# Kernel optimization log

Measured on AMD Instinct MI355X. Metric: run time of the kernel, lower is better.

Reference implementation:

```python
import jax, jax.numpy as jnp
import numpy as np


def setup_inputs() -> dict:
    key = jax.random.key(0)
    kq, kk, kv = jax.random.split(key, 3)
    B, M, QT, KVT, H = 2, 16, 2048, 2048, 128
    q = jax.random.normal(kq, (B, M, QT, H), dtype=jnp.float32)
    k = jax.random.normal(kk, (B, M, KVT, H), dtype=jnp.float32)
    v = jax.random.normal(kv, (B, M, KVT, H), dtype=jnp.float32)
    return {"q": q, "k": k, "v": v}


def reference(q, k, v):
    # QKBmm: broadcast-multiply + sum == einsum contraction over H.
    # NOTE: original module applies NO 1/sqrt(H) scaling.
    score = jnp.einsum("bmqh,bmkh->bmqk", q, k)  # [B,M,QT,KVT]
    score = jax.nn.softmax(score, axis=-1)
    # SVBmm: broadcast-multiply + sum over KVT.
    out = jnp.einsum("bmqk,bmkh->bmqh", score, v)  # [B,M,QT,H]
    return out
```

## Files before the change

### kernel.cpp

```cpp
#include <hip/hip_runtime.h>
#include <hip/hip_bf16.h>
#include <math.h>


#define HD     128
#define QTL    2048
#define KVTL   2048
#define NHEAD  32
#define KVBLK  64
#define NKT    (KVTL / KVBLK)
#define QBLKB  128
#define TILE_BYTES 32768
#define WS_NEEDED ((size_t)NHEAD * NKT * TILE_BYTES)

using f32x4  = __attribute__((ext_vector_type(4))) float;
using f32x16 = __attribute__((ext_vector_type(16))) float;
using f16x8  = __attribute__((ext_vector_type(8))) _Float16;
using f16x2  = __attribute__((ext_vector_type(2))) _Float16;
using i32x2  = __attribute__((ext_vector_type(2))) int;
using i32x4  = __attribute__((ext_vector_type(4))) int;
using bf16x8 = __attribute__((ext_vector_type(8))) __bf16;
using bf16x4 = __attribute__((ext_vector_type(4))) __bf16;

#define NK_CHUNK (NHEAD * NKT * 64 * 16)
#define NV_CHUNK (NHEAD * NKT * 8 * 128)

__global__ __launch_bounds__(256) void sdpa_prep(const float* __restrict__ kg,
                                                 const float* __restrict__ vg,
                                                 char* __restrict__ ws)
{
    const int idx = blockIdx.x * 256 + threadIdx.x;
    if (idx < NK_CHUNK) {
        const int s    = idx & 15;
        const int r    = (idx >> 4) & 63;
        const int kt   = (idx >> 10) & 31;
        const int head = idx >> 15;
        const int c    = s ^ (r & 15);
        const float* src = kg + ((size_t)head * KVTL + kt * 64 + r) * HD + c * 8;
        float4 a = *(const float4*)src;
        float4 b = *(const float4*)(src + 4);
        f16x8 h8;
        h8[0] = (_Float16)a.x; h8[1] = (_Float16)a.y;
        h8[2] = (_Float16)a.z; h8[3] = (_Float16)a.w;
        h8[4] = (_Float16)b.x; h8[5] = (_Float16)b.y;
        h8[6] = (_Float16)b.z; h8[7] = (_Float16)b.w;
        char* base = ws + (size_t)(head * NKT + kt) * TILE_BYTES;
        *(f16x8*)(base + r * 256 + s * 16) = h8;
    } else if (idx < NK_CHUNK + NV_CHUNK) {
        const int j    = idx - NK_CHUNK;
        const int h    = j & 127;
        const int c    = (j >> 7) & 7;
        const int kt   = (j >> 10) & 31;
        const int head = j >> 15;
        const int rr   = h & 63;
        const int u    = h >> 6;
        const int s    = (u * 8 + c) ^ (rr & 15);
        const float* src = vg + ((size_t)head * KVTL + kt * 64 + c * 8) * HD + h;
        f16x8 o;
        #pragma unroll
        for (int i = 0; i < 8; ++i)
            o[i] = (_Float16)src[(size_t)i * HD];
        char* base = ws + (size_t)(head * NKT + kt) * TILE_BYTES;
        *(f16x8*)(base + 16384 + rr * 256 + s * 16) = o;
    }
}

__device__ __forceinline__ void stage_tile(const char* __restrict__ g,
                                           char* lds, int t)
{
    #pragma unroll
    for (int j = 0; j < 8; ++j) {
        __builtin_amdgcn_global_load_lds(
            (const __attribute__((address_space(1))) void*)(g + j * 4096 + t * 16),
            (__attribute__((address_space(3))) void*)(lds + j * 4096 + t * 16),
            16, 0, 0);
    }
}

__global__ __launch_bounds__(256, 2) void sdpa_fwd(const float* __restrict__ qg,
                                                   const char* __restrict__ ws,
                                                   float* __restrict__ og)
{
    const int head  = blockIdx.y;
    const int qblk  = blockIdx.x * QBLKB;
    const float* qh = qg + (size_t)head * QTL * HD;
    const char*  wh = ws + (size_t)head * NKT * TILE_BYTES;

    const int t  = threadIdx.x;
    const int wv = t >> 6;
    const int l  = t & 63;
    const int lq = l & 31;
    const int hi = l >> 5;
    const int lm = l & 15;

    __shared__ __align__(16) char arena[65536];

    f16x8 qf[8];
    {
        const float* qrow = qh + (size_t)(qblk + wv * 32 + lq) * HD;
        #pragma unroll
        for (int hs = 0; hs < 8; ++hs) {
            float4 a = *(const float4*)(qrow + hs * 16 + hi * 8);
            float4 b = *(const float4*)(qrow + hs * 16 + hi * 8 + 4);
            f16x8 f;
            f[0] = (_Float16)a.x; f[1] = (_Float16)a.y;
            f[2] = (_Float16)a.z; f[3] = (_Float16)a.w;
            f[4] = (_Float16)b.x; f[5] = (_Float16)b.y;
            f[6] = (_Float16)b.z; f[7] = (_Float16)b.w;
            qf[hs] = f;
        }
    }

    f32x16 acc_o[4];
    #pragma unroll
    for (int ht = 0; ht < 4; ++ht)
        #pragma unroll
        for (int r = 0; r < 16; ++r) acc_o[ht][r] = 0.f;

    float m = -INFINITY, ln = 0.f;
    const float LOG2E = 1.4426950408889634f;

    stage_tile(wh, arena, t);
    __syncthreads();

    for (int kt = 0; kt < NKT; ++kt) {
        const int cur = kt & 1;
        char* base = arena + cur * 32768;
        if (kt + 1 < NKT)
            stage_tile(wh + (size_t)(kt + 1) * TILE_BYTES, arena + (cur ^ 1) * 32768, t);

        f32x16 acc_s[2];
        #pragma unroll
        for (int kk = 0; kk < 2; ++kk) {
            f32x16 acc;
            #pragma unroll
            for (int r = 0; r < 16; ++r) acc[r] = 0.f;
            #pragma unroll
            for (int hs = 0; hs < 8; ++hs) {
                const int off = (kk * 32 + lq) * 256 + (((hs * 2 + hi) ^ lm) * 16);
                f16x8 kf = *(const f16x8*)(base + off);
                acc = __builtin_amdgcn_mfma_f32_32x32x16_f16(kf, qf[hs], acc, 0, 0, 0);
            }
            acc_s[kk] = acc;
        }

        float pmax = -INFINITY;
        #pragma unroll
        for (int kk = 0; kk < 2; ++kk)
            #pragma unroll
            for (int r = 0; r < 16; ++r) pmax = fmaxf(pmax, acc_s[kk][r]);
        pmax = fmaxf(pmax, __shfl_xor(pmax, 32));

        if (!__all(pmax <= m + 8.0f)) {
            const float mnew = fmaxf(m, pmax);
            const float sc   = exp2f((m - mnew) * LOG2E);
            m = mnew; ln *= sc;
            #pragma unroll
            for (int ht = 0; ht < 4; ++ht)
                #pragma unroll
                for (int r = 0; r < 16; ++r) acc_o[ht][r] *= sc;
        }

        i32x4 fr[4];
        #pragma unroll
        for (int kk = 0; kk < 2; ++kk) {
            float p[16];
            float ps = 0.f;
            #pragma unroll
            for (int r = 0; r < 16; ++r) {
                p[r] = exp2f((acc_s[kk][r] - m) * LOG2E);
                ps += p[r];
            }
            ln += ps;
            int t01 = __builtin_bit_cast(int, __builtin_amdgcn_cvt_pkrtz(p[0],  p[1]));
            int t23 = __builtin_bit_cast(int, __builtin_amdgcn_cvt_pkrtz(p[2],  p[3]));
            int t45 = __builtin_bit_cast(int, __builtin_amdgcn_cvt_pkrtz(p[4],  p[5]));
            int t67 = __builtin_bit_cast(int, __builtin_amdgcn_cvt_pkrtz(p[6],  p[7]));
            int t89 = __builtin_bit_cast(int, __builtin_amdgcn_cvt_pkrtz(p[8],  p[9]));
            int tAB = __builtin_bit_cast(int, __builtin_amdgcn_cvt_pkrtz(p[10], p[11]));
            int tCD = __builtin_bit_cast(int, __builtin_amdgcn_cvt_pkrtz(p[12], p[13]));
            int tEF = __builtin_bit_cast(int, __builtin_amdgcn_cvt_pkrtz(p[14], p[15]));
            i32x2 sw;
            sw = __builtin_amdgcn_permlane32_swap(t01, t45, false, false);
            fr[2*kk][0] = sw[0]; fr[2*kk][2] = sw[1];
            sw = __builtin_amdgcn_permlane32_swap(t23, t67, false, false);
            fr[2*kk][1] = sw[0]; fr[2*kk][3] = sw[1];
            sw = __builtin_amdgcn_permlane32_swap(t89, tCD, false, false);
            fr[2*kk+1][0] = sw[0]; fr[2*kk+1][2] = sw[1];
            sw = __builtin_amdgcn_permlane32_swap(tAB, tEF, false, false);
            fr[2*kk+1][1] = sw[0]; fr[2*kk+1][3] = sw[1];
        }

        const char* Vb = base + 16384;
        #pragma unroll
        for (int ht = 0; ht < 4; ++ht) {
            #pragma unroll
            for (int ks = 0; ks < 4; ++ks) {
                const int off = ((ht & 1) * 32 + lq) * 256 +
                                ((((ht >> 1) * 8 + ks * 2 + hi) ^ lm) * 16);
                f16x8 vf = *(const f16x8*)(Vb + off);
                acc_o[ht] = __builtin_amdgcn_mfma_f32_32x32x16_f16(
                    vf, __builtin_bit_cast(f16x8, fr[ks]), acc_o[ht], 0, 0, 0);
            }
        }

        __syncthreads();
    }

    ln += __shfl_xor(ln, 32);
    const float inv = 1.f / ln;

    __syncthreads();
    const int qloc = wv * 32 + lq;
    #pragma unroll
    for (int ht = 0; ht < 4; ++ht) {
        #pragma unroll
        for (int r = 0; r < 4; ++r) {
            f32x4 v;
            v[0] = acc_o[ht][4*r+0] * inv;
            v[1] = acc_o[ht][4*r+1] * inv;
            v[2] = acc_o[ht][4*r+2] * inv;
            v[3] = acc_o[ht][4*r+3] * inv;
            const int slot = ht * 8 + 2 * r + hi;
            *(f32x4*)(arena + qloc * 512 + ((slot ^ lq) * 16)) = v;
        }
    }
    __syncthreads();
    {
        float* ob = og + (size_t)(head * QTL + qblk) * HD;
        #pragma unroll
        for (int j = 0; j < 16; ++j) {
            const int n  = j * 256 + t;
            const int qr = n >> 5;
            const int sl = n & 31;
            f32x4 v = *(const f32x4*)(arena + qr * 512 + ((sl ^ (qr & 31)) * 16));
            *(f32x4*)(ob + (size_t)qr * HD + sl * 4) = v;
        }
    }
}

__global__ __launch_bounds__(256) void sdpa_fwd_v1(const float* __restrict__ qg,
                                                   const float* __restrict__ kg,
                                                   const float* __restrict__ vg,
                                                   float* __restrict__ og)
{
    const int head  = blockIdx.y;
    const int qbase = blockIdx.x * 64;
    const float* qh = qg + (size_t)head * QTL * HD;
    const float* kh = kg + (size_t)head * KVTL * HD;
    const float* vh = vg + (size_t)head * KVTL * HD;
    float*       oh = og + (size_t)head * QTL * HD;

    const int t  = threadIdx.x;
    const int wv = t >> 6;
    const int l  = t & 63;
    const int lr = l & 15;
    const int lg = l >> 4;

    __shared__ __bf16 Kth[32][HD + 8];
    __shared__ __bf16 Ktl[32][HD + 8];
    __shared__ __bf16 Vt[HD][32 + 8];
    __shared__ __bf16 Pw[4][16][32 + 8];

    bf16x8 qfh[4], qfl[4];
    {
        const float* qrow = qh + (size_t)(qbase + wv * 16 + lr) * HD;
        #pragma unroll
        for (int ks = 0; ks < 4; ++ks) {
            bf16x8 fh, fl;
            #pragma unroll
            for (int i = 0; i < 8; ++i) {
                float x = qrow[ks * 32 + lg * 8 + i];
                __bf16 h = (__bf16)x;
                fh[i] = h;
                fl[i] = (__bf16)(x - (float)h);
            }
            qfh[ks] = fh; qfl[ks] = fl;
        }
    }

    f32x4 acc_o[8];
    #pragma unroll
    for (int h8 = 0; h8 < 8; ++h8) acc_o[h8] = (f32x4){0.f, 0.f, 0.f, 0.f};
    float mrow[4], lrow[4];
    #pragma unroll
    for (int r = 0; r < 4; ++r) { mrow[r] = -INFINITY; lrow[r] = 0.f; }
    const float LOG2E = 1.4426950408889634f;

    for (int kt = 0; kt < 64; ++kt) {
        const float* kbase = kh + (size_t)kt * 32 * HD;
        const float* vbase = vh + (size_t)kt * 32 * HD;
        __syncthreads();
        #pragma unroll
        for (int j = 0; j < 4; ++j) {
            const int e   = (j * 256 + t) * 4;
            const int row = e >> 7;
            const int col = e & 127;
            float4 f = *(const float4*)(kbase + e);
            bf16x4 h4, l4;
            h4[0] = (__bf16)f.x; l4[0] = (__bf16)(f.x - (float)h4[0]);
            h4[1] = (__bf16)f.y; l4[1] = (__bf16)(f.y - (float)h4[1]);
            h4[2] = (__bf16)f.z; l4[2] = (__bf16)(f.z - (float)h4[2]);
            h4[3] = (__bf16)f.w; l4[3] = (__bf16)(f.w - (float)h4[3]);
            *(bf16x4*)&Kth[row][col] = h4;
            *(bf16x4*)&Ktl[row][col] = l4;
        }
        #pragma unroll
        for (int j = 0; j < 4; ++j) {
            const int n     = t & 127;
            const int strip = (t >> 7) + 2 * j;
            bf16x4 b4;
            #pragma unroll
            for (int i = 0; i < 4; ++i)
                b4[i] = (__bf16)vbase[(size_t)(4 * strip + i) * HD + n];
            *(bf16x4*)&Vt[n][4 * strip] = b4;
        }
        __syncthreads();

        f32x4 acc_s[2];
        #pragma unroll
        for (int nt = 0; nt < 2; ++nt) {
            acc_s[nt] = (f32x4){0.f, 0.f, 0.f, 0.f};
            #pragma unroll
            for (int ks = 0; ks < 4; ++ks) {
                bf16x8 kh8 = *(const bf16x8*)&Kth[nt * 16 + lr][ks * 32 + lg * 8];
                bf16x8 kl8 = *(const bf16x8*)&Ktl[nt * 16 + lr][ks * 32 + lg * 8];
                acc_s[nt] = __builtin_amdgcn_mfma_f32_16x16x32_bf16(qfh[ks], kh8, acc_s[nt], 0, 0, 0);
                acc_s[nt] = __builtin_amdgcn_mfma_f32_16x16x32_bf16(qfl[ks], kh8, acc_s[nt], 0, 0, 0);
                acc_s[nt] = __builtin_amdgcn_mfma_f32_16x16x32_bf16(qfh[ks], kl8, acc_s[nt], 0, 0, 0);
            }
        }
        float p[2][4];
        #pragma unroll
        for (int r = 0; r < 4; ++r) {
            float vm = fmaxf(acc_s[0][r], acc_s[1][r]);
            vm = fmaxf(vm, __shfl_xor(vm, 1));
            vm = fmaxf(vm, __shfl_xor(vm, 2));
            vm = fmaxf(vm, __shfl_xor(vm, 4));
            vm = fmaxf(vm, __shfl_xor(vm, 8));
            const float mnew  = fmaxf(mrow[r], vm);
            const float scale = exp2f((mrow[r] - mnew) * LOG2E);
            mrow[r] = mnew;
            float ps = 0.f;
            #pragma unroll
            for (int nt = 0; nt < 2; ++nt) {
                float pe = exp2f((acc_s[nt][r] - mnew) * LOG2E);
                p[nt][r] = pe; ps += pe;
            }
            lrow[r] = lrow[r] * scale + ps;
            #pragma unroll
            for (int h8 = 0; h8 < 8; ++h8) acc_o[h8][r] *= scale;
        }
        #pragma unroll
        for (int nt = 0; nt < 2; ++nt)
            #pragma unroll
            for (int r = 0; r < 4; ++r)
                Pw[wv][lg * 4 + r][nt * 16 + lr] = (__bf16)p[nt][r];
        bf16x8 pf = *(const bf16x8*)&Pw[wv][lr][lg * 8];
        #pragma unroll
        for (int h8 = 0; h8 < 8; ++h8) {
            bf16x8 vf = *(const bf16x8*)&Vt[h8 * 16 + lr][lg * 8];
            acc_o[h8] = __builtin_amdgcn_mfma_f32_16x16x32_bf16(pf, vf, acc_o[h8], 0, 0, 0);
        }
    }
    float invl[4];
    #pragma unroll
    for (int r = 0; r < 4; ++r) {
        float s = lrow[r];
        s += __shfl_xor(s, 1);
        s += __shfl_xor(s, 2);
        s += __shfl_xor(s, 4);
        s += __shfl_xor(s, 8);
        invl[r] = 1.f / s;
    }
    float* ob = oh + (size_t)(qbase + wv * 16) * HD;
    #pragma unroll
    for (int h8 = 0; h8 < 8; ++h8)
        #pragma unroll
        for (int r = 0; r < 4; ++r)
            ob[(size_t)(lg * 4 + r) * HD + h8 * 16 + lr] = acc_o[h8][r] * invl[r];
}

extern "C" void kernel_launch(void* const* d_in, const int* in_sizes, int n_in,
                              void* d_out, int out_size, void* d_ws, size_t ws_size,
                              hipStream_t stream) {
    const float* q = (const float*)d_in[0];
    const float* k = (const float*)d_in[1];
    const float* v = (const float*)d_in[2];
    float* out = (float*)d_out;

    if (ws_size >= WS_NEEDED) {
        char* ws = (char*)d_ws;
        const int total_chunks = NK_CHUNK + NV_CHUNK;
        sdpa_prep<<<total_chunks / 256, 256, 0, stream>>>(k, v, ws);
        dim3 grid(QTL / QBLKB, NHEAD, 1);
        sdpa_fwd<<<grid, dim3(256, 1, 1), 0, stream>>>(q, ws, out);
    } else {
        dim3 grid(QTL / 64, NHEAD, 1);
        sdpa_fwd_v1<<<grid, dim3(256, 1, 1), 0, stream>>>(q, k, v, out);
    }
}
```

Measured before the change: 119.7 us.

## Use 512-thread blocks with 256 query rows sharing each staged KV tile

Doubles the query block per workgroup to 256 rows with 8 waves, so each K/V tile staged into LDS serves twice as many queries and global/LDS staging traffic per query halves. Adds s_setprio around the MFMA sections to favor matrix issue across waves, and splits the max/sum reductions into four independent chains for more ILP. The epilogue writes output in two halves through the 64KB arena. Grid halves to 8x32 blocks at one block per CU, which may reduce occupancy and load balance.

```diff
diff --git a/kernel.cpp b/kernel.cpp
--- a/kernel.cpp
+++ b/kernel.cpp
@@ -9,14 +9,13 @@
 #define NHEAD  32
 #define KVBLK  64
 #define NKT    (KVTL / KVBLK)
-#define QBLKB  128
+#define QBLKB  256
 #define TILE_BYTES 32768
 #define WS_NEEDED ((size_t)NHEAD * NKT * TILE_BYTES)
 
 using f32x4  = __attribute__((ext_vector_type(4))) float;
 using f32x16 = __attribute__((ext_vector_type(16))) float;
 using f16x8  = __attribute__((ext_vector_type(8))) _Float16;
-using f16x2  = __attribute__((ext_vector_type(2))) _Float16;
 using i32x2  = __attribute__((ext_vector_type(2))) int;
 using i32x4  = __attribute__((ext_vector_type(4))) int;
 using bf16x8 = __attribute__((ext_vector_type(8))) __bf16;
@@ -69,15 +68,15 @@
                                            char* lds, int t)
 {
     #pragma unroll
-    for (int j = 0; j < 8; ++j) {
+    for (int j = 0; j < 4; ++j) {
         __builtin_amdgcn_global_load_lds(
-            (const __attribute__((address_space(1))) void*)(g + j * 4096 + t * 16),
-            (__attribute__((address_space(3))) void*)(lds + j * 4096 + t * 16),
+            (const __attribute__((address_space(1))) void*)(g + j * 8192 + t * 16),
+            (__attribute__((address_space(3))) void*)(lds + j * 8192 + t * 16),
             16, 0, 0);
     }
 }
 
-__global__ __launch_bounds__(256, 2) void sdpa_fwd(const float* __restrict__ qg,
+__global__ __launch_bounds__(512, 1) void sdpa_fwd(const float* __restrict__ qg,
                                                    const char* __restrict__ ws,
                                                    float* __restrict__ og)
 {
@@ -130,6 +129,7 @@
             stage_tile(wh + (size_t)(kt + 1) * TILE_BYTES, arena + (cur ^ 1) * 32768, t);
 
         f32x16 acc_s[2];
+        __builtin_amdgcn_s_setprio(1);
         #pragma unroll
         for (int kk = 0; kk < 2; ++kk) {
             f32x16 acc;
@@ -143,12 +143,19 @@
             }
             acc_s[kk] = acc;
         }
-
-        float pmax = -INFINITY;
+        __builtin_amdgcn_s_setprio(0);
+
+        float pm0 = -INFINITY, pm1 = -INFINITY, pm2 = -INFINITY, pm3 = -INFINITY;
         #pragma unroll
         for (int kk = 0; kk < 2; ++kk)
             #pragma unroll
-            for (int r = 0; r < 16; ++r) pmax = fmaxf(pmax, acc_s[kk][r]);
+            for (int r = 0; r < 16; r += 4) {
+                pm0 = fmaxf(pm0, acc_s[kk][r + 0]);
+                pm1 = fmaxf(pm1, acc_s[kk][r + 1]);
+                pm2 = fmaxf(pm2, acc_s[kk][r + 2]);
+                pm3 = fmaxf(pm3, acc_s[kk][r + 3]);
+            }
+        float pmax = fmaxf(fmaxf(pm0, pm1), fmaxf(pm2, pm3));
         pmax = fmaxf(pmax, __shfl_xor(pmax, 32));
 
         if (!__all(pmax <= m + 8.0f)) {
@@ -165,13 +172,15 @@
         #pragma unroll
         for (int kk = 0; kk < 2; ++kk) {
             float p[16];
-            float ps = 0.f;
-            #pragma unroll
-            for (int r = 0; r < 16; ++r) {
-                p[r] = exp2f((acc_s[kk][r] - m) * LOG2E);
-                ps += p[r];
-            }
-            ln += ps;
+            float s0 = 0.f, s1 = 0.f, s2 = 0.f, s3 = 0.f;
+            #pragma unroll
+            for (int r = 0; r < 16; r += 4) {
+                p[r + 0] = exp2f((acc_s[kk][r + 0] - m) * LOG2E); s0 += p[r + 0];
+                p[r + 1] = exp2f((acc_s[kk][r + 1] - m) * LOG2E); s1 += p[r + 1];
+                p[r + 2] = exp2f((acc_s[kk][r + 2] - m) * LOG2E); s2 += p[r + 2];
+                p[r + 3] = exp2f((acc_s[kk][r + 3] - m) * LOG2E); s3 += p[r + 3];
+            }
+            ln += (s0 + s1) + (s2 + s3);
             int t01 = __builtin_bit_cast(int, __builtin_amdgcn_cvt_pkrtz(p[0],  p[1]));
             int t23 = __builtin_bit_cast(int, __builtin_amdgcn_cvt_pkrtz(p[2],  p[3]));
             int t45 = __builtin_bit_cast(int, __builtin_amdgcn_cvt_pkrtz(p[4],  p[5]));
@@ -192,6 +201,7 @@
         }
 
         const char* Vb = base + 16384;
+        __builtin_amdgcn_s_setprio(1);
         #pragma unroll
         for (int ht = 0; ht < 4; ++ht) {
             #pragma unroll
@@ -203,34 +213,39 @@
                     vf, __builtin_bit_cast(f16x8, fr[ks]), acc_o[ht], 0, 0, 0);
             }
         }
+        __builtin_amdgcn_s_setprio(0);
 
         __syncthreads();
     }
 
     ln += __shfl_xor(ln, 32);
     const float inv = 1.f / ln;
-
-    __syncthreads();
     const int qloc = wv * 32 + lq;
-    #pragma unroll
-    for (int ht = 0; ht < 4; ++ht) {
-        #pragma unroll
-        for (int r = 0; r < 4; ++r) {
-            f32x4 v;
-            v[0] = acc_o[ht][4*r+0] * inv;
-            v[1] = acc_o[ht][4*r+1] * inv;
-            v[2] = acc_o[ht][4*r+2] * inv;
-            v[3] = acc_o[ht][4*r+3] * inv;
-            const int slot = ht * 8 + 2 * r + hi;
-            *(f32x4*)(arena + qloc * 512 + ((slot ^ lq) * 16)) = v;
-        }
-    }
-    __syncthreads();
-    {
-        float* ob = og + (size_t)(head * QTL + qblk) * HD;
-        #pragma unroll
-        for (int j = 0; j < 16; ++j) {
-            const int n  = j * 256 + t;
+
+    #pragma unroll
+    for (int half = 0; half < 2; ++half) {
+        __syncthreads();
+        if ((wv >> 2) == half) {
+            const int lrow = qloc - half * 128;
+            #pragma unroll
+            for (int ht = 0; ht < 4; ++ht) {
+                #pragma unroll
+                for (int r = 0; r < 4; ++r) {
+                    f32x4 v;
+                    v[0] = acc_o[ht][4*r+0] * inv;
+                    v[1] = acc_o[ht][4*r+1] * inv;
+                    v[2] = acc_o[ht][4*r+2] * inv;
+                    v[3] = acc_o[ht][4*r+3] * inv;
+                    const int slot = ht * 8 + 2 * r + hi;
+                    *(f32x4*)(arena + lrow * 512 + ((slot ^ lq) * 16)) = v;
+                }
+            }
+        }
+        __syncthreads();
+        float* ob = og + (size_t)(head * QTL + qblk + half * 128) * HD;
+        #pragma unroll
+        for (int j = 0; j < 8; ++j) {
+            const int n  = j * 512 + t;
             const int qr = n >> 5;
             const int sl = n & 31;
             f32x4 v = *(const f32x4*)(arena + qr * 512 + ((sl ^ (qr & 31)) * 16));
@@ -394,7 +409,7 @@
         const int total_chunks = NK_CHUNK + NV_CHUNK;
         sdpa_prep<<<total_chunks / 256, 256, 0, stream>>>(k, v, ws);
         dim3 grid(QTL / QBLKB, NHEAD, 1);
-        sdpa_fwd<<<grid, dim3(256, 1, 1), 0, stream>>>(q, ws, out);
+        sdpa_fwd<<<grid, dim3(512, 1, 1), 0, stream>>>(q, ws, out);
     } else {
         dim3 grid(QTL / 64, NHEAD, 1);
         sdpa_fwd_v1<<<grid, dim3(256, 1, 1), 0, stream>>>(q, k, v, out);
```

Result: faster. 114.8 us (median of 2 runs) (-4.1%).

## Halve KV tile to 32 rows to fit four blocks per CU

Applied to the files above, without the earlier changes.

Shrinks the KV tile from 64 to 32 rows, so the double-buffered LDS arena drops from 64KB to 32KB, and raises launch bounds to 4 blocks per CU. The K/V workspace layout in the prep kernel is re-derived for the smaller tile, and the output epilogue is split into two halves so it fits the smaller arena. It also adds s_setprio around the MFMA sections and splits the max and sum reductions into parallel partial chains. The aim is more resident waves to hide latency, at the cost of twice as many loop iterations and barriers, more online-softmax rescale checks, and tighter register limits that may spill.

```diff
diff --git a/kernel.cpp b/kernel.cpp
--- a/kernel.cpp
+++ b/kernel.cpp
@@ -7,23 +7,22 @@
 #define QTL    2048
 #define KVTL   2048
 #define NHEAD  32
-#define KVBLK  64
+#define KVBLK  32
 #define NKT    (KVTL / KVBLK)
 #define QBLKB  128
-#define TILE_BYTES 32768
+#define TILE_BYTES 16384
 #define WS_NEEDED ((size_t)NHEAD * NKT * TILE_BYTES)
 
 using f32x4  = __attribute__((ext_vector_type(4))) float;
 using f32x16 = __attribute__((ext_vector_type(16))) float;
 using f16x8  = __attribute__((ext_vector_type(8))) _Float16;
-using f16x2  = __attribute__((ext_vector_type(2))) _Float16;
 using i32x2  = __attribute__((ext_vector_type(2))) int;
 using i32x4  = __attribute__((ext_vector_type(4))) int;
 using bf16x8 = __attribute__((ext_vector_type(8))) __bf16;
 using bf16x4 = __attribute__((ext_vector_type(4))) __bf16;
 
-#define NK_CHUNK (NHEAD * NKT * 64 * 16)
-#define NV_CHUNK (NHEAD * NKT * 8 * 128)
+#define NK_CHUNK (NHEAD * NKT * 32 * 16)
+#define NV_CHUNK (NHEAD * NKT * 32 * 16)
 
 __global__ __launch_bounds__(256) void sdpa_prep(const float* __restrict__ kg,
                                                  const float* __restrict__ vg,
@@ -32,11 +31,11 @@
     const int idx = blockIdx.x * 256 + threadIdx.x;
     if (idx < NK_CHUNK) {
         const int s    = idx & 15;
-        const int r    = (idx >> 4) & 63;
-        const int kt   = (idx >> 10) & 31;
+        const int r    = (idx >> 4) & 31;
+        const int kt   = (idx >> 9) & 63;
         const int head = idx >> 15;
         const int c    = s ^ (r & 15);
-        const float* src = kg + ((size_t)head * KVTL + kt * 64 + r) * HD + c * 8;
+        const float* src = kg + ((size_t)head * KVTL + kt * 32 + r) * HD + c * 8;
         float4 a = *(const float4*)src;
         float4 b = *(const float4*)(src + 4);
         f16x8 h8;
@@ -48,20 +47,20 @@
         *(f16x8*)(base + r * 256 + s * 16) = h8;
     } else if (idx < NK_CHUNK + NV_CHUNK) {
         const int j    = idx - NK_CHUNK;
-        const int h    = j & 127;
-        const int c    = (j >> 7) & 7;
-        const int kt   = (j >> 10) & 31;
+        const int s    = j & 15;
+        const int r    = (j >> 4) & 31;
+        const int kt   = (j >> 9) & 63;
         const int head = j >> 15;
-        const int rr   = h & 63;
-        const int u    = h >> 6;
-        const int s    = (u * 8 + c) ^ (rr & 15);
-        const float* src = vg + ((size_t)head * KVTL + kt * 64 + c * 8) * HD + h;
+        const int m    = s ^ (r & 15);
+        const int u    = m >> 2;
+        const int c    = m & 3;
+        const float* src = vg + ((size_t)head * KVTL + kt * 32 + c * 8) * HD + (u * 32 + r);
         f16x8 o;
         #pragma unroll
         for (int i = 0; i < 8; ++i)
             o[i] = (_Float16)src[(size_t)i * HD];
         char* base = ws + (size_t)(head * NKT + kt) * TILE_BYTES;
-        *(f16x8*)(base + 16384 + rr * 256 + s * 16) = o;
+        *(f16x8*)(base + 8192 + r * 256 + s * 16) = o;
     }
 }
 
@@ -69,7 +68,7 @@
                                            char* lds, int t)
 {
     #pragma unroll
-    for (int j = 0; j < 8; ++j) {
+    for (int j = 0; j < 4; ++j) {
         __builtin_amdgcn_global_load_lds(
             (const __attribute__((address_space(1))) void*)(g + j * 4096 + t * 16),
             (__attribute__((address_space(3))) void*)(lds + j * 4096 + t * 16),
@@ -77,7 +76,7 @@
     }
 }
 
-__global__ __launch_bounds__(256, 2) void sdpa_fwd(const float* __restrict__ qg,
+__global__ __launch_bounds__(256, 4) void sdpa_fwd(const float* __restrict__ qg,
                                                    const char* __restrict__ ws,
                                                    float* __restrict__ og)
 {
@@ -93,7 +92,7 @@
     const int hi = l >> 5;
     const int lm = l & 15;
 
-    __shared__ __align__(16) char arena[65536];
+    __shared__ __align__(16) char arena[2 * TILE_BYTES];
 
     f16x8 qf[8];
     {
@@ -123,32 +122,35 @@
     stage_tile(wh, arena, t);
     __syncthreads();
 
+    #pragma unroll 2
     for (int kt = 0; kt < NKT; ++kt) {
         const int cur = kt & 1;
-        char* base = arena + cur * 32768;
+        char* base = arena + cur * TILE_BYTES;
         if (kt + 1 < NKT)
-            stage_tile(wh + (size_t)(kt + 1) * TILE_BYTES, arena + (cur ^ 1) * 32768, t);
-
-        f32x16 acc_s[2];
-        #pragma unroll
-        for (int kk = 0; kk < 2; ++kk) {
-            f32x16 acc;
-            #pragma unroll
-            for (int r = 0; r < 16; ++r) acc[r] = 0.f;
-            #pragma unroll
-            for (int hs = 0; hs < 8; ++hs) {
-                const int off = (kk * 32 + lq) * 256 + (((hs * 2 + hi) ^ lm) * 16);
-                f16x8 kf = *(const f16x8*)(base + off);
-                acc = __builtin_amdgcn_mfma_f32_32x32x16_f16(kf, qf[hs], acc, 0, 0, 0);
-            }
-            acc_s[kk] = acc;
-        }
-
-        float pmax = -INFINITY;
-        #pragma unroll
-        for (int kk = 0; kk < 2; ++kk)
-            #pragma unroll
-            for (int r = 0; r < 16; ++r) pmax = fmaxf(pmax, acc_s[kk][r]);
+            stage_tile(wh + (size_t)(kt + 1) * TILE_BYTES,
+                       arena + (cur ^ 1) * TILE_BYTES, t);
+
+        f32x16 acc_s;
+        #pragma unroll
+        for (int r = 0; r < 16; ++r) acc_s[r] = 0.f;
+        __builtin_amdgcn_s_setprio(1);
+        #pragma unroll
+        for (int hs = 0; hs < 8; ++hs) {
+            const int off = lq * 256 + ((((hs << 1) | hi) ^ lm) * 16);
+            f16x8 kf = *(const f16x8*)(base + off);
+            acc_s = __builtin_amdgcn_mfma_f32_32x32x16_f16(kf, qf[hs], acc_s, 0, 0, 0);
+        }
+        __builtin_amdgcn_s_setprio(0);
+
+        float pm0 = fmaxf(acc_s[0],  acc_s[1]);
+        float pm1 = fmaxf(acc_s[2],  acc_s[3]);
+        float pm2 = fmaxf(acc_s[4],  acc_s[5]);
+        float pm3 = fmaxf(acc_s[6],  acc_s[7]);
+        pm0 = fmaxf(pm0, fmaxf(acc_s[8],  acc_s[9]));
+        pm1 = fmaxf(pm1, fmaxf(acc_s[10], acc_s[11]));
+        pm2 = fmaxf(pm2, fmaxf(acc_s[12], acc_s[13]));
+        pm3 = fmaxf(pm3, fmaxf(acc_s[14], acc_s[15]));
+        float pmax = fmaxf(fmaxf(pm0, pm1), fmaxf(pm2, pm3));
         pmax = fmaxf(pmax, __shfl_xor(pmax, 32));
 
         if (!__all(pmax <= m + 8.0f)) {
@@ -161,17 +163,20 @@
                 for (int r = 0; r < 16; ++r) acc_o[ht][r] *= sc;
         }
 
-        i32x4 fr[4];
-        #pragma unroll
-        for (int kk = 0; kk < 2; ++kk) {
-            float p[16];
-            float ps = 0.f;
-            #pragma unroll
-            for (int r = 0; r < 16; ++r) {
-                p[r] = exp2f((acc_s[kk][r] - m) * LOG2E);
-                ps += p[r];
-            }
-            ln += ps;
+        float p[16];
+        {
+            float s0 = 0.f, s1 = 0.f, s2 = 0.f, s3 = 0.f;
+            #pragma unroll
+            for (int r = 0; r < 16; r += 4) {
+                p[r + 0] = exp2f((acc_s[r + 0] - m) * LOG2E); s0 += p[r + 0];
+                p[r + 1] = exp2f((acc_s[r + 1] - m) * LOG2E); s1 += p[r + 1];
+                p[r + 2] = exp2f((acc_s[r + 2] - m) * LOG2E); s2 += p[r + 2];
+                p[r + 3] = exp2f((acc_s[r + 3] - m) * LOG2E); s3 += p[r + 3];
+            }
+            ln += (s0 + s1) + (s2 + s3);
+        }
+        i32x4 fr[2];
+        {
             int t01 = __builtin_bit_cast(int, __builtin_amdgcn_cvt_pkrtz(p[0],  p[1]));
             int t23 = __builtin_bit_cast(int, __builtin_amdgcn_cvt_pkrtz(p[2],  p[3]));
             int t45 = __builtin_bit_cast(int, __builtin_amdgcn_cvt_pkrtz(p[4],  p[5]));
@@ -182,27 +187,29 @@
             int tEF = __builtin_bit_cast(int, __builtin_amdgcn_cvt_pkrtz(p[14], p[15]));
             i32x2 sw;
             sw = __builtin_amdgcn_permlane32_swap(t01, t45, false, false);
-            fr[2*kk][0] = sw[0]; fr[2*kk][2] = sw[1];
+            fr[0][0] = sw[0]; fr[0][2] = sw[1];
             sw = __builtin_amdgcn_permlane32_swap(t23, t67, false, false);
-            fr[2*kk][1] = sw[0]; fr[2*kk][3] = sw[1];
+            fr[0][1] = sw[0]; fr[0][3] = sw[1];
             sw = __builtin_amdgcn_permlane32_swap(t89, tCD, false, false);
-            fr[2*kk+1][0] = sw[0]; fr[2*kk+1][2] = sw[1];
+            fr[1][0] = sw[0]; fr[1][2] = sw[1];
             sw = __builtin_amdgcn_permlane32_swap(tAB, tEF, false, false);
-            fr[2*kk+1][1] = sw[0]; fr[2*kk+1][3] = sw[1];
-        }
-
-        const char* Vb = base + 16384;
+            fr[1][1] = sw[0]; fr[1][3] = sw[1];
+        }
+
+        const char* Vb = base + 8192;
+        __builtin_amdgcn_s_setprio(1);
         #pragma unroll
         for (int ht = 0; ht < 4; ++ht) {
             #pragma unroll
-            for (int ks = 0; ks < 4; ++ks) {
-                const int off = ((ht & 1) * 32 + lq) * 256 +
-                                ((((ht >> 1) * 8 + ks * 2 + hi) ^ lm) * 16);
+            for (int ks = 0; ks < 2; ++ks) {
+                const int off = lq * 256 +
+                                ((((ht << 2) | (ks << 1) | hi) ^ lm) * 16);
                 f16x8 vf = *(const f16x8*)(Vb + off);
                 acc_o[ht] = __builtin_amdgcn_mfma_f32_32x32x16_f16(
                     vf, __builtin_bit_cast(f16x8, fr[ks]), acc_o[ht], 0, 0, 0);
             }
         }
+        __builtin_amdgcn_s_setprio(0);
 
         __syncthreads();
     }
@@ -210,26 +217,29 @@
     ln += __shfl_xor(ln, 32);
     const float inv = 1.f / ln;
 
-    __syncthreads();
-    const int qloc = wv * 32 + lq;
-    #pragma unroll
-    for (int ht = 0; ht < 4; ++ht) {
-        #pragma unroll
-        for (int r = 0; r < 4; ++r) {
-            f32x4 v;
-            v[0] = acc_o[ht][4*r+0] * inv;
-            v[1] = acc_o[ht][4*r+1] * inv;
-            v[2] = acc_o[ht][4*r+2] * inv;
-            v[3] = acc_o[ht][4*r+3] * inv;
-            const int slot = ht * 8 + 2 * r + hi;
-            *(f32x4*)(arena + qloc * 512 + ((slot ^ lq) * 16)) = v;
-        }
-    }
-    __syncthreads();
-    {
-        float* ob = og + (size_t)(head * QTL + qblk) * HD;
-        #pragma unroll
-        for (int j = 0; j < 16; ++j) {
+    #pragma unroll
+    for (int half = 0; half < 2; ++half) {
+        __syncthreads();
+        if ((wv >> 1) == half) {
+            const int lrow = (wv & 1) * 32 + lq;
+            #pragma unroll
+            for (int ht = 0; ht < 4; ++ht) {
+                #pragma unroll
+                for (int rr = 0; rr < 4; ++rr) {
+                    f32x4 v;
+                    v[0] = acc_o[ht][4*rr+0] * inv;
+                    v[1] = acc_o[ht][4*rr+1] * inv;
+                    v[2] = acc_o[ht][4*rr+2] * inv;
+                    v[3] = acc_o[ht][4*rr+3] * inv;
+                    const int slot = ht * 8 + 2 * rr + hi;
+                    *(f32x4*)(arena + lrow * 512 + ((slot ^ lq) * 16)) = v;
+                }
+            }
+        }
+        __syncthreads();
+        float* ob = og + (size_t)(head * QTL + qblk + half * 64) * HD;
+        #pragma unroll
+        for (int j = 0; j < 8; ++j) {
             const int n  = j * 256 + t;
             const int qr = n >> 5;
             const int sl = n & 31;
```

Result: slower. 183.8 us (+53.5%).

## Software-pipeline QK of next tile with softmax/PV of previous tile

Applied to the files above, without the earlier changes.

Splits K and V staging into separate double-buffered halves and restructures the loop so the QK^T MFMAs for tile kt are issued alongside the softmax and PV of tile kt-1. The goal is to overlap exp/VALU work with matrix-core work and to let V loads arrive later than K loads. It also adds s_setprio around the MFMA sections and splits the max and sum reductions into multiple accumulators for ILP. This raises register pressure from holding two score tiles live, which could cause spills under the 2-waves launch bound.

```diff
diff --git a/kernel.cpp b/kernel.cpp
--- a/kernel.cpp
+++ b/kernel.cpp
@@ -16,7 +16,6 @@
 using f32x4  = __attribute__((ext_vector_type(4))) float;
 using f32x16 = __attribute__((ext_vector_type(16))) float;
 using f16x8  = __attribute__((ext_vector_type(8))) _Float16;
-using f16x2  = __attribute__((ext_vector_type(2))) _Float16;
 using i32x2  = __attribute__((ext_vector_type(2))) int;
 using i32x4  = __attribute__((ext_vector_type(4))) int;
 using bf16x8 = __attribute__((ext_vector_type(8))) __bf16;
@@ -65,11 +64,11 @@
     }
 }
 
-__device__ __forceinline__ void stage_tile(const char* __restrict__ g,
+__device__ __forceinline__ void stage_half(const char* __restrict__ g,
                                            char* lds, int t)
 {
     #pragma unroll
-    for (int j = 0; j < 8; ++j) {
+    for (int j = 0; j < 4; ++j) {
         __builtin_amdgcn_global_load_lds(
             (const __attribute__((address_space(1))) void*)(g + j * 4096 + t * 16),
             (__attribute__((address_space(3))) void*)(lds + j * 4096 + t * 16),
@@ -94,6 +93,10 @@
     const int lm = l & 15;
 
     __shared__ __align__(16) char arena[65536];
+    char* const KbA = arena;
+    char* const KbB = arena + 16384;
+    char* const VbA = arena + 32768;
+    char* const VbB = arena + 49152;
 
     f16x8 qf[8];
     {
@@ -120,35 +123,16 @@
     float m = -INFINITY, ln = 0.f;
     const float LOG2E = 1.4426950408889634f;
 
-    stage_tile(wh, arena, t);
-    __syncthreads();
-
-    for (int kt = 0; kt < NKT; ++kt) {
-        const int cur = kt & 1;
-        char* base = arena + cur * 32768;
-        if (kt + 1 < NKT)
-            stage_tile(wh + (size_t)(kt + 1) * TILE_BYTES, arena + (cur ^ 1) * 32768, t);
-
-        f32x16 acc_s[2];
-        #pragma unroll
-        for (int kk = 0; kk < 2; ++kk) {
-            f32x16 acc;
-            #pragma unroll
-            for (int r = 0; r < 16; ++r) acc[r] = 0.f;
-            #pragma unroll
-            for (int hs = 0; hs < 8; ++hs) {
-                const int off = (kk * 32 + lq) * 256 + (((hs * 2 + hi) ^ lm) * 16);
-                f16x8 kf = *(const f16x8*)(base + off);
-                acc = __builtin_amdgcn_mfma_f32_32x32x16_f16(kf, qf[hs], acc, 0, 0, 0);
-            }
-            acc_s[kk] = acc;
-        }
-
-        float pmax = -INFINITY;
-        #pragma unroll
-        for (int kk = 0; kk < 2; ++kk)
-            #pragma unroll
-            for (int r = 0; r < 16; ++r) pmax = fmaxf(pmax, acc_s[kk][r]);
+    auto finish_pv = [&](const f32x16& s0, const f32x16& s1, const char* Vp) {
+        float pm0 = -INFINITY, pm1 = -INFINITY, pm2 = -INFINITY, pm3 = -INFINITY;
+        #pragma unroll
+        for (int r = 0; r < 16; r += 4) {
+            pm0 = fmaxf(pm0, fmaxf(s0[r + 0], s1[r + 0]));
+            pm1 = fmaxf(pm1, fmaxf(s0[r + 1], s1[r + 1]));
+            pm2 = fmaxf(pm2, fmaxf(s0[r + 2], s1[r + 2]));
+            pm3 = fmaxf(pm3, fmaxf(s0[r + 3], s1[r + 3]));
+        }
+        float pmax = fmaxf(fmaxf(pm0, pm1), fmaxf(pm2, pm3));
         pmax = fmaxf(pmax, __shfl_xor(pmax, 32));
 
         if (!__all(pmax <= m + 8.0f)) {
@@ -164,14 +148,17 @@
         i32x4 fr[4];
         #pragma unroll
         for (int kk = 0; kk < 2; ++kk) {
+            const f32x16& s = kk ? s1 : s0;
             float p[16];
-            float ps = 0.f;
-            #pragma unroll
-            for (int r = 0; r < 16; ++r) {
-                p[r] = exp2f((acc_s[kk][r] - m) * LOG2E);
-                ps += p[r];
-            }
-            ln += ps;
+            float a0 = 0.f, a1 = 0.f, a2 = 0.f, a3 = 0.f;
+            #pragma unroll
+            for (int r = 0; r < 16; r += 4) {
+                p[r + 0] = exp2f((s[r + 0] - m) * LOG2E); a0 += p[r + 0];
+                p[r + 1] = exp2f((s[r + 1] - m) * LOG2E); a1 += p[r + 1];
+                p[r + 2] = exp2f((s[r + 2] - m) * LOG2E); a2 += p[r + 2];
+                p[r + 3] = exp2f((s[r + 3] - m) * LOG2E); a3 += p[r + 3];
+            }
+            ln += (a0 + a1) + (a2 + a3);
             int t01 = __builtin_bit_cast(int, __builtin_amdgcn_cvt_pkrtz(p[0],  p[1]));
             int t23 = __builtin_bit_cast(int, __builtin_amdgcn_cvt_pkrtz(p[2],  p[3]));
             int t45 = __builtin_bit_cast(int, __builtin_amdgcn_cvt_pkrtz(p[4],  p[5]));
@@ -191,21 +178,67 @@
             fr[2*kk+1][1] = sw[0]; fr[2*kk+1][3] = sw[1];
         }
 
-        const char* Vb = base + 16384;
+        __builtin_amdgcn_s_setprio(1);
         #pragma unroll
         for (int ht = 0; ht < 4; ++ht) {
             #pragma unroll
             for (int ks = 0; ks < 4; ++ks) {
                 const int off = ((ht & 1) * 32 + lq) * 256 +
                                 ((((ht >> 1) * 8 + ks * 2 + hi) ^ lm) * 16);
-                f16x8 vf = *(const f16x8*)(Vb + off);
+                f16x8 vf = *(const f16x8*)(Vp + off);
                 acc_o[ht] = __builtin_amdgcn_mfma_f32_32x32x16_f16(
                     vf, __builtin_bit_cast(f16x8, fr[ks]), acc_o[ht], 0, 0, 0);
             }
         }
-
+        __builtin_amdgcn_s_setprio(0);
+    };
+
+    auto qk = [&](const char* Kc, f32x16& d0, f32x16& d1) {
+        __builtin_amdgcn_s_setprio(1);
+        #pragma unroll
+        for (int kk = 0; kk < 2; ++kk) {
+            f32x16 acc;
+            #pragma unroll
+            for (int r = 0; r < 16; ++r) acc[r] = 0.f;
+            #pragma unroll
+            for (int hs = 0; hs < 8; ++hs) {
+                const int off = (kk * 32 + lq) * 256 + (((hs * 2 + hi) ^ lm) * 16);
+                f16x8 kf = *(const f16x8*)(Kc + off);
+                acc = __builtin_amdgcn_mfma_f32_32x32x16_f16(kf, qf[hs], acc, 0, 0, 0);
+            }
+            if (kk) d1 = acc; else d0 = acc;
+        }
+        __builtin_amdgcn_s_setprio(0);
+    };
+
+    stage_half(wh, KbA, t);
+    __syncthreads();
+
+    f32x16 sprev0, sprev1;
+    stage_half(wh + TILE_BYTES, KbB, t);
+    stage_half(wh + 16384, VbA, t);
+    qk(KbA, sprev0, sprev1);
+    __syncthreads();
+
+    for (int kt = 1; kt < NKT; ++kt) {
+        const char* Kc = (kt & 1) ? KbB : KbA;
+        char*       Kn = (kt & 1) ? KbA : KbB;
+        char*       Vc = (kt & 1) ? VbB : VbA;
+        const char* Vp = (kt & 1) ? VbA : VbB;
+
+        if (kt + 1 < NKT)
+            stage_half(wh + (size_t)(kt + 1) * TILE_BYTES, Kn, t);
+        stage_half(wh + (size_t)kt * TILE_BYTES + 16384, Vc, t);
+
+        f32x16 snew0, snew1;
+        qk(Kc, snew0, snew1);
+        finish_pv(sprev0, sprev1, Vp);
+
+        sprev0 = snew0; sprev1 = snew1;
         __syncthreads();
     }
+
+    finish_pv(sprev0, sprev1, VbB);
 
     ln += __shfl_xor(ln, 32);
     const float inv = 1.f / ln;
```

Result: slower. 123.4 us (+3.1%).
